# Optimization experiments

Hardware: AMD Instinct MI355X
Metric: run time of the kernel (lower is better)

The kernel has to match this reference:

```python
import jax, jax.numpy as jnp
import numpy as np

EMBED_DIM = 1024
NUM_HEADS = 16
D_K = EMBED_DIM // NUM_HEADS


def setup_inputs() -> dict:
    key = jax.random.key(0)
    ks = jax.random.split(key, 9)
    B, T, C = 4, 2048, EMBED_DIM
    s = 1.0 / np.sqrt(C)
    inp = {
        "x": jax.random.normal(ks[0], (B, T, C), dtype=jnp.float32),
        "Wq": jax.random.uniform(ks[1], (C, C), jnp.float32, -s, s),
        "bq": jax.random.uniform(ks[2], (C,), jnp.float32, -s, s),
        "Wk": jax.random.uniform(ks[3], (C, C), jnp.float32, -s, s),
        "bk": jax.random.uniform(ks[4], (C,), jnp.float32, -s, s),
        "Wv": jax.random.uniform(ks[5], (C, C), jnp.float32, -s, s),
        "bv": jax.random.uniform(ks[6], (C,), jnp.float32, -s, s),
        "Wo": jax.random.uniform(ks[7], (C, C), jnp.float32, -s, s),
        "bo": jax.random.uniform(ks[8], (C,), jnp.float32, -s, s),
    }
    return inp


def reference(x, Wq, bq, Wk, bk, Wv, bv, Wo, bo):
    B, T, C = x.shape
    H, Dk = NUM_HEADS, D_K
    # torch Linear: y = x @ W.T + b
    def proj(W, b):
        y = jnp.einsum('btc,dc->btd', x, W) + b
        return y.reshape(B, T, H, Dk).transpose(0, 2, 1, 3)  # [B,H,T,Dk]
    q = proj(Wq, bq)
    k = proj(Wk, bk)
    v = proj(Wv, bv)
    scores = jnp.einsum('bhtd,bhsd->bhts', q, k) / jnp.sqrt(jnp.float32(Dk))
    attn = jax.nn.softmax(scores, axis=-1)
    ctx = jnp.einsum('bhts,bhsd->bhtd', attn, v)
    ctx = ctx.transpose(0, 2, 1, 3).reshape(B, T, C)
    return jnp.einsum('btc,dc->btd', ctx, Wo) + bo
```

## Files before the change

### kernel.cpp

```cpp
#include <hip/hip_runtime.h>
#include <hip/hip_bf16.h>
#include <cstdint>

using u16 = unsigned short;
typedef __attribute__((ext_vector_type(8))) short short8;
typedef __attribute__((ext_vector_type(8))) _Float16 f16x8;
typedef __attribute__((ext_vector_type(4))) float floatx4;

#define MFMA16(a, b, c) __builtin_amdgcn_mfma_f32_16x16x32_bf16((a), (b), (c), 0, 0, 0)
#define MFMAH(a, b, c)  __builtin_amdgcn_mfma_f32_16x16x32_f16((a), (b), (c), 0, 0, 0)

#define GLL(gp, lp) __builtin_amdgcn_global_load_lds( \
    (const __attribute__((address_space(1))) unsigned int*)(gp), \
    (__attribute__((address_space(3))) unsigned int*)(lp), 16, 0, 0)

__device__ __forceinline__ u16 f2bf(float f) {
    union { float f; unsigned u; } v; v.f = f;
    return (u16)((v.u + 0x7FFFu + ((v.u >> 16) & 1u)) >> 16);
}
__device__ __forceinline__ u16 f2h(float f) {
    _Float16 h = (_Float16)f;
    return __builtin_bit_cast(u16, h);
}
__device__ __forceinline__ unsigned cvt_pk_bf16(float lo, float hi) {
    unsigned r;
    asm("v_cvt_pk_bf16_f32 %0, %1, %2" : "=v"(r) : "v"(lo), "v"(hi));
    return r;
}
__device__ __forceinline__ float fast_exp2(float x) {
#if __has_builtin(__builtin_amdgcn_exp2f)
    return __builtin_amdgcn_exp2f(x);
#else
    float r; asm("v_exp_f32 %0, %1" : "=v"(r) : "v"(x)); return r;
#endif
}
__device__ __forceinline__ float fast_rcp(float x) {
#if __has_builtin(__builtin_amdgcn_rcpf)
    return __builtin_amdgcn_rcpf(x);
#else
    float r; asm("v_rcp_f32 %0, %1" : "=v"(r) : "v"(x)); return r;
#endif
}

__global__ void cast_x_f16(const float* __restrict__ src, u16* __restrict__ dst, int n4) {
    int idx = blockIdx.x * blockDim.x + threadIdx.x;
    int stride = gridDim.x * blockDim.x;
    for (int i = idx; i < n4; i += stride) {
        float4 v = reinterpret_cast<const float4*>(src)[i];
        reinterpret_cast<ushort4*>(dst)[i] =
            make_ushort4(f2h(v.x), f2h(v.y), f2h(v.z), f2h(v.w));
    }
}

__global__ void cast_w_f16(const float* q, const float* k, const float* v, const float* o,
                           u16* q16, u16* k16, u16* v16, u16* o16, int n4) {
    const float* src; u16* dst;
    switch (blockIdx.y) {
        case 0:  src = q; dst = q16; break;
        case 1:  src = k; dst = k16; break;
        case 2:  src = v; dst = v16; break;
        default: src = o; dst = o16; break;
    }
    int idx = blockIdx.x * blockDim.x + threadIdx.x;
    int stride = gridDim.x * blockDim.x;
    for (int i = idx; i < n4; i += stride) {
        float4 w = reinterpret_cast<const float4*>(src)[i];
        reinterpret_cast<ushort4*>(dst)[i] =
            make_ushort4(f2h(w.x), f2h(w.y), f2h(w.z), f2h(w.w));
    }
}

template <int TERMS>
__global__ __launch_bounds__(256) void gemm_f16(
    const u16* __restrict__ A16, const u16* __restrict__ A16l,
    const u16* __restrict__ B16, const float* __restrict__ bias,
    u16* __restrict__ out16, float* __restrict__ outf, int mode, float scale) {
    constexpr int NT = TERMS + 1;
    __shared__ __align__(16) char ldsb[NT * 8192];

    int flat = blockIdx.x + (blockIdx.y << 6);
    int swz = (flat & 7) * 64 + (flat >> 3);
    const int m0 = ((swz >> 6) * 8 + ((swz >> 3) & 7)) << 7;
    const int n0 = (swz & 7) << 7;

    const int t = threadIdx.x, lane = t & 63, w = t >> 6;
    const int c = lane & 15, g = lane >> 4;
    const int wm = w & 1, wn = w >> 1;

    floatx4 zero = {0.f, 0.f, 0.f, 0.f};
    floatx4 acc[4][4];
#pragma unroll
    for (int mf = 0; mf < 4; ++mf)
#pragma unroll
        for (int nf = 0; nf < 4; ++nf) acc[mf][nf] = zero;

    const u16* gsrc[NT];
    gsrc[0] = A16 + (size_t)m0 * 1024;
    if (TERMS == 2) gsrc[1] = A16l + (size_t)m0 * 1024;
    gsrc[NT - 1] = B16 + (size_t)n0 * 1024;

    int dst_db[2 * NT];
    size_t src_el[2 * NT];
#pragma unroll
    for (int j = 0; j < 2 * NT; ++j) {
        int db = t * 16 + j * 4096;
        int local = db & 8191;
        int row = local >> 6;
        int colsw = (local & 63) ^ (((local >> 7) & 3) << 4);
        dst_db[j] = db;
        src_el[j] = (size_t)row * 1024 + (colsw >> 1);
    }

    int offA[4], offB[4];
#pragma unroll
    for (int f = 0; f < 4; ++f) {
        int rA = wm * 64 + f * 16 + c;
        offA[f] = rA * 64 + ((g * 16) ^ (((rA >> 1) & 3) << 4));
        int rB = wn * 64 + f * 16 + c;
        offB[f] = (TERMS * 8192) + rB * 64 + ((g * 16) ^ (((rB >> 1) & 3) << 4));
    }

    for (int k0 = 0; k0 < 1024; k0 += 32) {
        __syncthreads();
#pragma unroll
        for (int j = 0; j < 2 * NT; ++j)
            GLL(gsrc[j >> 1] + src_el[j] + k0, ldsb + dst_db[j]);
        __syncthreads();

        f16x8 a[4], al[4], b[4];
#pragma unroll
        for (int f = 0; f < 4; ++f) {
            a[f] = *reinterpret_cast<const f16x8*>(ldsb + offA[f]);
            if (TERMS == 2)
                al[f] = *reinterpret_cast<const f16x8*>(ldsb + 8192 + offA[f]);
            b[f] = *reinterpret_cast<const f16x8*>(ldsb + offB[f]);
        }
#pragma unroll
        for (int mf = 0; mf < 4; ++mf)
#pragma unroll
            for (int nf = 0; nf < 4; ++nf) {
                acc[mf][nf] = MFMAH(a[mf], b[nf], acc[mf][nf]);
                if (TERMS == 2) acc[mf][nf] = MFMAH(al[mf], b[nf], acc[mf][nf]);
            }
    }

#pragma unroll
    for (int nf = 0; nf < 4; ++nf) {
        int col = n0 + wn * 64 + nf * 16 + c;
        float bv = bias[col];
#pragma unroll
        for (int mf = 0; mf < 4; ++mf) {
            int rb = m0 + wm * 64 + mf * 16 + 4 * g;
            if (mode == 2) {
#pragma unroll
                for (int i = 0; i < 4; ++i)
                    outf[(size_t)(rb + i) * 1024 + col] = (acc[mf][nf][i] + bv) * scale;
            } else {
                int b = rb >> 11, tt = rb & 2047, h = col >> 6, dk = col & 63;
                if (mode == 0) {
#pragma unroll
                    for (int i = 0; i < 4; ++i)
                        out16[((size_t)(b * 16 + h) * 2048 + tt + i) * 64 + dk] =
                            f2bf((acc[mf][nf][i] + bv) * scale);
                } else {
                    ushort4 pk;
                    pk.x = f2bf((acc[mf][nf][0] + bv) * scale);
                    pk.y = f2bf((acc[mf][nf][1] + bv) * scale);
                    pk.z = f2bf((acc[mf][nf][2] + bv) * scale);
                    pk.w = f2bf((acc[mf][nf][3] + bv) * scale);
                    int k64 = tt & 63, q = k64 >> 4, sub = (k64 >> 2) & 3;
                    int pos = ((q >> 1) << 5) + (sub << 3) + ((q & 1) << 2);
                    *reinterpret_cast<ushort4*>(
                        out16 + ((size_t)(b * 16 + h) * 64 + dk) * 2048 +
                        (tt & ~63) + pos) = pk;
                }
            }
        }
    }
}

__global__ __launch_bounds__(512) void attn_flash(
    const u16* __restrict__ Q, const u16* __restrict__ K, const u16* __restrict__ Vt,
    u16* __restrict__ ctx) {
    __shared__ __align__(16) char kv_lds[2][16384];

    int flat = blockIdx.x + (blockIdx.y << 4);
    int swz = (flat & 7) * 128 + (flat >> 3);
    const int q0 = (swz & 15) << 7;
    const int bh = swz >> 4;

    const int lane = threadIdx.x & 63, w = threadIdx.x >> 6;
    const int c = lane & 15, g = lane >> 4;

    const u16* qrow = Q + ((size_t)bh * 2048 + q0 + w * 16 + c) * 64;
    short8 qf0 = *reinterpret_cast<const short8*>(qrow + g * 8);
    short8 qf1 = *reinterpret_cast<const short8*>(qrow + 32 + g * 8);

    const bool isK = (w < 4);
    const char* sptr = isK ? (const char*)(K + (size_t)bh * 2048 * 64)
                           : (const char*)(Vt + (size_t)bh * 64 * 2048);
    const int sadv = isK ? 8192 : 128;
    size_t src_off[2];
    int dst_off[2];
#pragma unroll
    for (int j = 0; j < 2; ++j) {
        int base = (w & 3) * 2048 + j * 1024 + lane * 16;
        int row = base >> 7, col = (base & 127) ^ ((row & 7) << 4);
        if (isK) { dst_off[j] = base;        src_off[j] = (size_t)row * 128  + col; }
        else     { dst_off[j] = 8192 + base; src_off[j] = (size_t)row * 4096 + col; }
    }

    const int sw = (c & 7) << 4;
    const int abase0 = c * 128 + ((g * 16) ^ sw);
    const int abase1 = c * 128 + ((64 + g * 16) ^ sw);

    short8 ones;
#pragma unroll
    for (int e = 0; e < 8; ++e) ones[e] = (short)0x3F80;

    floatx4 zero = {0.f, 0.f, 0.f, 0.f};
    floatx4 acc[4] = {zero, zero, zero, zero};
    floatx4 acc5 = zero;

#define STAGE_TO(BUF) do { \
    GLL(sptr + src_off[0], (char*)kv_lds + (BUF) * 16384 + dst_off[0]); \
    GLL(sptr + src_off[1], (char*)kv_lds + (BUF) * 16384 + dst_off[1]); \
    sptr += sadv; } while (0)

#define TILE(BUF) do { \
    const char* kbL = (const char*)kv_lds + (BUF) * 16384; \
    floatx4 st[4]; \
    __builtin_amdgcn_s_setprio(1); \
    _Pragma("unroll") \
    for (int kf = 0; kf < 4; ++kf) { \
        short8 k0 = *reinterpret_cast<const short8*>(kbL + kf * 2048 + abase0); \
        short8 k1 = *reinterpret_cast<const short8*>(kbL + kf * 2048 + abase1); \
        st[kf] = MFMA16(k1, qf1, MFMA16(k0, qf0, zero)); \
    } \
    __builtin_amdgcn_s_setprio(0); \
    float p[4][4]; \
    _Pragma("unroll") \
    for (int kf = 0; kf < 4; ++kf) \
        _Pragma("unroll") \
        for (int i = 0; i < 4; ++i) p[kf][i] = fast_exp2(st[kf][i]); \
    union { unsigned u[4]; short8 s; } pa0, pa1; \
    pa0.u[0] = cvt_pk_bf16(p[0][0], p[0][1]); \
    pa0.u[1] = cvt_pk_bf16(p[0][2], p[0][3]); \
    pa0.u[2] = cvt_pk_bf16(p[1][0], p[1][1]); \
    pa0.u[3] = cvt_pk_bf16(p[1][2], p[1][3]); \
    pa1.u[0] = cvt_pk_bf16(p[2][0], p[2][1]); \
    pa1.u[1] = cvt_pk_bf16(p[2][2], p[2][3]); \
    pa1.u[2] = cvt_pk_bf16(p[3][0], p[3][1]); \
    pa1.u[3] = cvt_pk_bf16(p[3][2], p[3][3]); \
    __builtin_amdgcn_s_setprio(1); \
    acc5 = MFMA16(pa0.s, ones, acc5); \
    acc5 = MFMA16(pa1.s, ones, acc5); \
    _Pragma("unroll") \
    for (int nt = 0; nt < 4; ++nt) { \
        short8 vf0 = *reinterpret_cast<const short8*>(kbL + 8192 + nt * 2048 + abase0); \
        short8 vf1 = *reinterpret_cast<const short8*>(kbL + 8192 + nt * 2048 + abase1); \
        acc[nt] = MFMA16(pa1.s, vf1, MFMA16(pa0.s, vf0, acc[nt])); \
    } \
    __builtin_amdgcn_s_setprio(0); } while (0)

    STAGE_TO(0);
    for (int t = 0; t < 32; t += 2) {
        __syncthreads();
        STAGE_TO(1);
        TILE(0);
        __syncthreads();
        if (t + 2 < 32) STAGE_TO(0);
        TILE(1);
    }
#undef STAGE_TO
#undef TILE

    const int b = bh >> 4, h = bh & 15;
    float rl[4];
#pragma unroll
    for (int i = 0; i < 4; ++i) rl[i] = fast_rcp(acc5[i]);
#pragma unroll
    for (int nt = 0; nt < 4; ++nt) {
#pragma unroll
        for (int i = 0; i < 4; ++i) {
            int tt = q0 + w * 16 + 4 * g + i;
            size_t idx = ((size_t)b * 2048 + tt) * 1024 + h * 64 + nt * 16 + c;
            ctx[idx] = f2h(acc[nt][i] * rl[i]);
        }
    }
}

extern "C" void kernel_launch(void* const* d_in, const int* in_sizes, int n_in,
                              void* d_out, int out_size, void* d_ws, size_t ws_size,
                              hipStream_t stream) {
    if (n_in < 9) return;
    const float* x  = (const float*)d_in[0];
    const float* Wq = (const float*)d_in[1];
    const float* bq = (const float*)d_in[2];
    const float* Wk = (const float*)d_in[3];
    const float* bk = (const float*)d_in[4];
    const float* Wv = (const float*)d_in[5];
    const float* bv = (const float*)d_in[6];
    const float* Wo = (const float*)d_in[7];
    const float* bo = (const float*)d_in[8];
    float* out = (float*)d_out;

    const size_t NX = 8192ull * 1024ull;
    const size_t NW = 1024ull * 1024ull;
    u16* p = (u16*)d_ws;
    u16* x16  = p; p += NX;
    u16* Wq16 = p; p += NW;
    u16* Wk16 = p; p += NW;
    u16* Wv16 = p; p += NW;
    u16* Wo16 = p; p += NW;
    u16* Qb   = p; p += NX;
    u16* Kb   = p; p += NX;
    u16* Vtb  = p; p += NX;
    u16* cx   = p; p += NX;
    if ((size_t)((char*)p - (char*)d_ws) > ws_size) return;

    dim3 blk(256);
    cast_x_f16<<<dim3(2048), blk, 0, stream>>>(x, x16, (int)(NX / 4));
    cast_w_f16<<<dim3(256, 4), blk, 0, stream>>>(
        Wq, Wk, Wv, Wo, Wq16, Wk16, Wv16, Wo16, (int)(NW / 4));

    dim3 ggrid(64, 8);
    const float qscale = 0.125f * 1.44269504088896f;
    gemm_f16<1><<<ggrid, blk, 0, stream>>>(x16, x16, Wq16, bq, Qb, nullptr, 0, qscale);
    gemm_f16<1><<<ggrid, blk, 0, stream>>>(x16, x16, Wk16, bk, Kb, nullptr, 0, 1.0f);
    gemm_f16<1><<<ggrid, blk, 0, stream>>>(x16, x16, Wv16, bv, Vtb, nullptr, 1, 1.0f);

    attn_flash<<<dim3(16, 64), dim3(512), 0, stream>>>(Qb, Kb, Vtb, cx);

    gemm_f16<1><<<ggrid, blk, 0, stream>>>(cx, cx, Wo16, bo, nullptr, out, 2, 1.0f);
}
```

Measured before the change: 198.3 us.

## Fuse QKV projections into one launch and software-pipeline attention PV with next QK

The three Q/K/V projection GEMMs now run as a single launch with blockIdx.z choosing the weight, bias and output layout, so each GEMM pass is no longer limited to 512 blocks and launch overhead drops. The attention loop is restructured so that the P·V MFMAs of the previous tile are issued alongside the QK^T MFMAs of the current tile, with V fragments held in registers across phases. This is meant to hide the exp and convert latency behind matrix work. The cost is higher register pressure from the extra V fragments and P buffers, which could lower occupancy.

```diff
diff --git a/kernel.cpp b/kernel.cpp
--- a/kernel.cpp
+++ b/kernel.cpp
@@ -70,14 +70,10 @@
     }
 }
 
-template <int TERMS>
-__global__ __launch_bounds__(256) void gemm_f16(
-    const u16* __restrict__ A16, const u16* __restrict__ A16l,
-    const u16* __restrict__ B16, const float* __restrict__ bias,
-    u16* __restrict__ out16, float* __restrict__ outf, int mode, float scale) {
-    constexpr int NT = TERMS + 1;
-    __shared__ __align__(16) char ldsb[NT * 8192];
-
+__device__ __forceinline__ void gemm_core(
+    const u16* __restrict__ A16, const u16* __restrict__ B16,
+    const float* __restrict__ bias, u16* __restrict__ out16,
+    float* __restrict__ outf, int mode, float scale, char* ldsb) {
     int flat = blockIdx.x + (blockIdx.y << 6);
     int swz = (flat & 7) * 64 + (flat >> 3);
     const int m0 = ((swz >> 6) * 8 + ((swz >> 3) & 7)) << 7;
@@ -94,15 +90,12 @@
 #pragma unroll
         for (int nf = 0; nf < 4; ++nf) acc[mf][nf] = zero;
 
-    const u16* gsrc[NT];
-    gsrc[0] = A16 + (size_t)m0 * 1024;
-    if (TERMS == 2) gsrc[1] = A16l + (size_t)m0 * 1024;
-    gsrc[NT - 1] = B16 + (size_t)n0 * 1024;
-
-    int dst_db[2 * NT];
-    size_t src_el[2 * NT];
-#pragma unroll
-    for (int j = 0; j < 2 * NT; ++j) {
+    const u16* gsrc[2] = {A16 + (size_t)m0 * 1024, B16 + (size_t)n0 * 1024};
+
+    int dst_db[4];
+    size_t src_el[4];
+#pragma unroll
+    for (int j = 0; j < 4; ++j) {
         int db = t * 16 + j * 4096;
         int local = db & 8191;
         int row = local >> 6;
@@ -117,31 +110,27 @@
         int rA = wm * 64 + f * 16 + c;
         offA[f] = rA * 64 + ((g * 16) ^ (((rA >> 1) & 3) << 4));
         int rB = wn * 64 + f * 16 + c;
-        offB[f] = (TERMS * 8192) + rB * 64 + ((g * 16) ^ (((rB >> 1) & 3) << 4));
+        offB[f] = 8192 + rB * 64 + ((g * 16) ^ (((rB >> 1) & 3) << 4));
     }
 
     for (int k0 = 0; k0 < 1024; k0 += 32) {
         __syncthreads();
 #pragma unroll
-        for (int j = 0; j < 2 * NT; ++j)
+        for (int j = 0; j < 4; ++j)
             GLL(gsrc[j >> 1] + src_el[j] + k0, ldsb + dst_db[j]);
         __syncthreads();
 
-        f16x8 a[4], al[4], b[4];
+        f16x8 a[4], b[4];
 #pragma unroll
         for (int f = 0; f < 4; ++f) {
             a[f] = *reinterpret_cast<const f16x8*>(ldsb + offA[f]);
-            if (TERMS == 2)
-                al[f] = *reinterpret_cast<const f16x8*>(ldsb + 8192 + offA[f]);
             b[f] = *reinterpret_cast<const f16x8*>(ldsb + offB[f]);
         }
 #pragma unroll
         for (int mf = 0; mf < 4; ++mf)
 #pragma unroll
-            for (int nf = 0; nf < 4; ++nf) {
+            for (int nf = 0; nf < 4; ++nf)
                 acc[mf][nf] = MFMAH(a[mf], b[nf], acc[mf][nf]);
-                if (TERMS == 2) acc[mf][nf] = MFMAH(al[mf], b[nf], acc[mf][nf]);
-            }
     }
 
 #pragma unroll
@@ -179,6 +168,24 @@
     }
 }
 
+__global__ __launch_bounds__(256) void gemm_qkv(
+    const u16* __restrict__ x16,
+    const u16* __restrict__ Wq, const u16* __restrict__ Wk, const u16* __restrict__ Wv,
+    const float* __restrict__ bq, const float* __restrict__ bk, const float* __restrict__ bv,
+    u16* __restrict__ Qb, u16* __restrict__ Kb, u16* __restrict__ Vtb, float qscale) {
+    __shared__ __align__(16) char lds[16384];
+    if (blockIdx.z == 0)      gemm_core(x16, Wq, bq, Qb,  nullptr, 0, qscale, lds);
+    else if (blockIdx.z == 1) gemm_core(x16, Wk, bk, Kb,  nullptr, 0, 1.0f, lds);
+    else                      gemm_core(x16, Wv, bv, Vtb, nullptr, 1, 1.0f, lds);
+}
+
+__global__ __launch_bounds__(256) void gemm_o(
+    const u16* __restrict__ cx, const u16* __restrict__ Wo,
+    const float* __restrict__ bo, float* __restrict__ out) {
+    __shared__ __align__(16) char lds[16384];
+    gemm_core(cx, Wo, bo, nullptr, out, 2, 1.0f, lds);
+}
+
 __global__ __launch_bounds__(512) void attn_flash(
     const u16* __restrict__ Q, const u16* __restrict__ K, const u16* __restrict__ Vt,
     u16* __restrict__ ctx) {
@@ -222,12 +229,18 @@
     floatx4 acc[4] = {zero, zero, zero, zero};
     floatx4 acc5 = zero;
 
+    union pa_t { unsigned u[4]; short8 s; };
+    pa_t paA0, paA1, paB0, paB1;
+    short8 vrA[8], vrB[8];
+
 #define STAGE_TO(BUF) do { \
     GLL(sptr + src_off[0], (char*)kv_lds + (BUF) * 16384 + dst_off[0]); \
     GLL(sptr + src_off[1], (char*)kv_lds + (BUF) * 16384 + dst_off[1]); \
     sptr += sadv; } while (0)
 
-#define TILE(BUF) do { \
+#define PHASE(BUF, PAc0, PAc1, VRc, PAp0, PAp1, VRp, DO_PV, DO_STAGE, SBUF) do { \
+    __syncthreads(); \
+    if (DO_STAGE) STAGE_TO(SBUF); \
     const char* kbL = (const char*)kv_lds + (BUF) * 16384; \
     floatx4 st[4]; \
     __builtin_amdgcn_s_setprio(1); \
@@ -237,43 +250,48 @@
         short8 k1 = *reinterpret_cast<const short8*>(kbL + kf * 2048 + abase1); \
         st[kf] = MFMA16(k1, qf1, MFMA16(k0, qf0, zero)); \
     } \
+    if (DO_PV) { \
+        acc5 = MFMA16(PAp0.s, ones, acc5); \
+        acc5 = MFMA16(PAp1.s, ones, acc5); \
+        _Pragma("unroll") \
+        for (int nt = 0; nt < 4; ++nt) \
+            acc[nt] = MFMA16(PAp1.s, VRp[nt + 4], MFMA16(PAp0.s, VRp[nt], acc[nt])); \
+    } \
     __builtin_amdgcn_s_setprio(0); \
+    _Pragma("unroll") \
+    for (int nt = 0; nt < 4; ++nt) { \
+        VRc[nt]     = *reinterpret_cast<const short8*>(kbL + 8192 + nt * 2048 + abase0); \
+        VRc[nt + 4] = *reinterpret_cast<const short8*>(kbL + 8192 + nt * 2048 + abase1); \
+    } \
     float p[4][4]; \
     _Pragma("unroll") \
     for (int kf = 0; kf < 4; ++kf) \
         _Pragma("unroll") \
         for (int i = 0; i < 4; ++i) p[kf][i] = fast_exp2(st[kf][i]); \
-    union { unsigned u[4]; short8 s; } pa0, pa1; \
-    pa0.u[0] = cvt_pk_bf16(p[0][0], p[0][1]); \
-    pa0.u[1] = cvt_pk_bf16(p[0][2], p[0][3]); \
-    pa0.u[2] = cvt_pk_bf16(p[1][0], p[1][1]); \
-    pa0.u[3] = cvt_pk_bf16(p[1][2], p[1][3]); \
-    pa1.u[0] = cvt_pk_bf16(p[2][0], p[2][1]); \
-    pa1.u[1] = cvt_pk_bf16(p[2][2], p[2][3]); \
-    pa1.u[2] = cvt_pk_bf16(p[3][0], p[3][1]); \
-    pa1.u[3] = cvt_pk_bf16(p[3][2], p[3][3]); \
-    __builtin_amdgcn_s_setprio(1); \
-    acc5 = MFMA16(pa0.s, ones, acc5); \
-    acc5 = MFMA16(pa1.s, ones, acc5); \
-    _Pragma("unroll") \
-    for (int nt = 0; nt < 4; ++nt) { \
-        short8 vf0 = *reinterpret_cast<const short8*>(kbL + 8192 + nt * 2048 + abase0); \
-        short8 vf1 = *reinterpret_cast<const short8*>(kbL + 8192 + nt * 2048 + abase1); \
-        acc[nt] = MFMA16(pa1.s, vf1, MFMA16(pa0.s, vf0, acc[nt])); \
-    } \
-    __builtin_amdgcn_s_setprio(0); } while (0)
+    PAc0.u[0] = cvt_pk_bf16(p[0][0], p[0][1]); \
+    PAc0.u[1] = cvt_pk_bf16(p[0][2], p[0][3]); \
+    PAc0.u[2] = cvt_pk_bf16(p[1][0], p[1][1]); \
+    PAc0.u[3] = cvt_pk_bf16(p[1][2], p[1][3]); \
+    PAc1.u[0] = cvt_pk_bf16(p[2][0], p[2][1]); \
+    PAc1.u[1] = cvt_pk_bf16(p[2][2], p[2][3]); \
+    PAc1.u[2] = cvt_pk_bf16(p[3][0], p[3][1]); \
+    PAc1.u[3] = cvt_pk_bf16(p[3][2], p[3][3]); \
+    } while (0)
 
     STAGE_TO(0);
-    for (int t = 0; t < 32; t += 2) {
-        __syncthreads();
-        STAGE_TO(1);
-        TILE(0);
-        __syncthreads();
-        if (t + 2 < 32) STAGE_TO(0);
-        TILE(1);
-    }
+    PHASE(0, paA0, paA1, vrA, paB0, paB1, vrB, 0, 1, 1);
+    for (int it = 0; it < 15; ++it) {
+        PHASE(1, paB0, paB1, vrB, paA0, paA1, vrA, 1, 1, 0);
+        PHASE(0, paA0, paA1, vrA, paB0, paB1, vrB, 1, 1, 1);
+    }
+    PHASE(1, paB0, paB1, vrB, paA0, paA1, vrA, 1, 0, 0);
+    acc5 = MFMA16(paB0.s, ones, acc5);
+    acc5 = MFMA16(paB1.s, ones, acc5);
+#pragma unroll
+    for (int nt = 0; nt < 4; ++nt)
+        acc[nt] = MFMA16(paB1.s, vrB[nt + 4], MFMA16(paB0.s, vrB[nt], acc[nt]));
 #undef STAGE_TO
-#undef TILE
+#undef PHASE
 
     const int b = bh >> 4, h = bh & 15;
     float rl[4];
@@ -324,13 +342,11 @@
     cast_w_f16<<<dim3(256, 4), blk, 0, stream>>>(
         Wq, Wk, Wv, Wo, Wq16, Wk16, Wv16, Wo16, (int)(NW / 4));
 
-    dim3 ggrid(64, 8);
     const float qscale = 0.125f * 1.44269504088896f;
-    gemm_f16<1><<<ggrid, blk, 0, stream>>>(x16, x16, Wq16, bq, Qb, nullptr, 0, qscale);
-    gemm_f16<1><<<ggrid, blk, 0, stream>>>(x16, x16, Wk16, bk, Kb, nullptr, 0, 1.0f);
-    gemm_f16<1><<<ggrid, blk, 0, stream>>>(x16, x16, Wv16, bv, Vtb, nullptr, 1, 1.0f);
+    gemm_qkv<<<dim3(64, 8, 3), blk, 0, stream>>>(
+        x16, Wq16, Wk16, Wv16, bq, bk, bv, Qb, Kb, Vtb, qscale);
 
     attn_flash<<<dim3(16, 64), dim3(512), 0, stream>>>(Qb, Kb, Vtb, cx);
 
-    gemm_f16<1><<<ggrid, blk, 0, stream>>>(cx, cx, Wo16, bo, nullptr, out, 2, 1.0f);
-}
+    gemm_o<<<dim3(64, 8), blk, 0, stream>>>(cx, Wo16, bo, out);
+}
```

Measured after the change: 179.9 us. 9.3% less time.
